# Optimization experiments

Hardware: AMD Instinct MI355X
Metric: run time of the kernel (lower is better)

Reference implementation:

```python
import jax, jax.numpy as jnp
import numpy as np


def rotate_half(x):
    d = x.shape[-1] // 2
    return jnp.concatenate([-x[..., d:], x[..., :d]], axis=-1)


def setup_inputs() -> dict:
    key = jax.random.key(0)
    ks = jax.random.split(key, 8)
    B, T, C, H = 2, 2048, 2048, 16
    hd = C // H
    x = jax.random.normal(ks[0], (B, T, C), dtype=jnp.float32)
    # realistic RoPE tables
    inv_freq = 1.0 / (10000.0 ** (jnp.arange(0, hd, 2, dtype=jnp.float32) / hd))
    t = jnp.arange(T, dtype=jnp.float32)
    freqs = jnp.einsum('t,f->tf', t, inv_freq)
    emb = jnp.concatenate([freqs, freqs], axis=-1)  # [T, hd]
    cos = jnp.cos(emb)
    sin = jnp.sin(emb)
    mask = jnp.tril(jnp.ones((T, T), dtype=bool))[None, None]  # causal [1,1,T,T]
    s = C ** -0.5
    Wq = jax.random.normal(ks[1], (C, C), dtype=jnp.float32) * s
    Wk = jax.random.normal(ks[2], (C, C), dtype=jnp.float32) * s
    Wv = jax.random.normal(ks[3], (C, C), dtype=jnp.float32) * s
    Wo = jax.random.normal(ks[4], (C, C), dtype=jnp.float32) * s
    return {"x": x, "cos": cos, "sin": sin, "mask": mask,
            "Wq": Wq, "Wk": Wk, "Wv": Wv, "Wo": Wo}


def reference(x, cos, sin, mask, Wq, Wk, Wv, Wo):
    B, T, C = x.shape
    H = 16
    hd = C // H
    scale = hd ** -0.5
    # projections: torch Linear stores W as [out,in], y = x @ W^T
    def proj(W):
        return jnp.einsum('btc,dc->btd', x, W).reshape(B, T, H, hd).transpose(0, 2, 1, 3)
    q, k, v = proj(Wq), proj(Wk), proj(Wv)  # [B,H,T,hd]
    c = cos[None, None]  # [1,1,T,hd]
    s = sin[None, None]
    q = q * c + rotate_half(q) * s
    k = k * c + rotate_half(k) * s
    attn = jnp.einsum('bhqd,bhkd->bhqk', q, k) * scale
    attn = jnp.where(mask, attn, -jnp.inf)
    attn = jax.nn.softmax(attn, axis=-1)
    out = jnp.einsum('bhqk,bhkd->bhqd', attn, v)
    out = out.transpose(0, 2, 1, 3).reshape(B, T, C)
    return jnp.einsum('btc,dc->btd', out, Wo)
```

## Files before the change

### kernel.cpp

```cpp
#include <hip/hip_runtime.h>
#include <cstdint>

typedef __bf16 bf16_t;
typedef __bf16 bf16x8 __attribute__((ext_vector_type(8)));
typedef __bf16 bf16x4 __attribute__((ext_vector_type(4)));
typedef float  f32x4  __attribute__((ext_vector_type(4)));

#define BB 2
#define TT 2048
#define CC 2048
#define HH 16
#define HD 128

static __device__ __forceinline__ void async_copy16(const void* gp, void* lp) {
  __builtin_amdgcn_global_load_lds(
      (const __attribute__((address_space(1))) void*)(uintptr_t)gp,
      (__attribute__((address_space(3))) void*)(uint32_t)(uintptr_t)lp,
      16, 0, 0);
}

__global__ __launch_bounds__(256)
void cast_all(const float* __restrict__ x, const float* __restrict__ wq,
              const float* __restrict__ wk, const float* __restrict__ wv,
              const float* __restrict__ wo, bf16_t* __restrict__ xb,
              bf16_t* __restrict__ wq_b) {
  const int NX4 = (BB * TT * CC) / 4;
  const int NW4 = (CC * CC) / 4;
  int i = blockIdx.x * 256 + threadIdx.x;
  const float* s;
  bf16_t* d;
  int off;
  if (i < NX4) {
    s = x; d = xb; off = i;
  } else {
    int j = i - NX4;
    int w = j >> 20;
    off = j & (NW4 - 1);
    s = (w == 0) ? wq : (w == 1) ? wk : (w == 2) ? wv : wo;
    d = wq_b + (size_t)w * (CC * CC);
  }
  float4 v = ((const float4*)s)[off];
  bf16x4 o;
  o[0] = (bf16_t)v.x; o[1] = (bf16_t)v.y; o[2] = (bf16_t)v.z; o[3] = (bf16_t)v.w;
  ((bf16x4*)d)[off] = o;
}

template <int MODE>
__global__ __launch_bounds__(256)
void gemm_bt(const bf16_t* __restrict__ A, const bf16_t* __restrict__ Bw,
             void* __restrict__ C0, void* __restrict__ C1, void* __restrict__ C2,
             int Kdim, int Ndim) {
  __shared__ __align__(16) char smem[128 * 136 * 2];
  bf16_t* As = (bf16_t*)smem;
  bf16_t* Bs = (bf16_t*)(smem + 16384);
  const int tid  = threadIdx.x;
  const int wave = tid >> 6, lane = tid & 63;
  const int quad = lane >> 4, l16 = lane & 15;
  const int m0 = blockIdx.y * 128, n0 = blockIdx.x * 128;
  const int wm = (wave >> 1) * 64, wn = (wave & 1) * 64;

  f32x4 acc[4][4] = {};

  const int srow = lane >> 3;
  const int scol = (((lane & 7) ^ srow) & 7) * 8;
  const int swz  = (l16 & 7) * 8;

  for (int k0 = 0; k0 < Kdim; k0 += 64) {
#pragma unroll
    for (int i = 0; i < 4; ++i) {
      int chunk = wave * 4 + i;
      int row = chunk * 8 + srow;
      async_copy16(A + (size_t)(m0 + row) * Kdim + k0 + scol, As + chunk * 512);
    }
#pragma unroll
    for (int i = 0; i < 4; ++i) {
      int chunk = wave * 4 + i;
      int row = chunk * 8 + srow;
      async_copy16(Bw + (size_t)(n0 + row) * Kdim + k0 + scol, Bs + chunk * 512);
    }
    __syncthreads();
#pragma unroll
    for (int kk = 0; kk < 64; kk += 32) {
      const int koff = (kk + quad * 8) ^ swz;
      bf16x8 af[4], bfr[4];
#pragma unroll
      for (int i = 0; i < 4; ++i)
        af[i] = *(const bf16x8*)&As[(wm + i * 16 + l16) * 64 + koff];
#pragma unroll
      for (int j = 0; j < 4; ++j)
        bfr[j] = *(const bf16x8*)&Bs[(wn + j * 16 + l16) * 64 + koff];
#pragma unroll
      for (int i = 0; i < 4; ++i)
#pragma unroll
        for (int j = 0; j < 4; ++j)
          acc[i][j] = __builtin_amdgcn_mfma_f32_16x16x32_bf16(af[i], bfr[j], acc[i][j], 0, 0, 0);
    }
    __syncthreads();
  }

  if (MODE == 0) {
#pragma unroll
    for (int i = 0; i < 4; ++i)
#pragma unroll
      for (int j = 0; j < 4; ++j) {
        int gcol = n0 + wn + j * 16 + l16;
#pragma unroll
        for (int r = 0; r < 4; ++r) {
          int grow = m0 + wm + i * 16 + quad * 4 + r;
          ((float*)C0)[(size_t)grow * Ndim + gcol] = acc[i][j][r];
        }
      }
  } else {
    const int proj = n0 >> 11;
    const int h = (n0 & (CC - 1)) >> 7;
    if (proj < 2) {
      bf16_t* dst = (bf16_t*)(proj == 0 ? C0 : C1);
#pragma unroll
      for (int i = 0; i < 4; ++i)
#pragma unroll
        for (int j = 0; j < 4; ++j) {
          int d = wn + j * 16 + l16;
#pragma unroll
          for (int r = 0; r < 4; ++r) {
            int grow = m0 + wm + i * 16 + quad * 4 + r;
            int b = grow >> 11, t = grow & (TT - 1);
            dst[(((size_t)(b * HH + h) * TT + t) * HD) + d] = (bf16_t)acc[i][j][r];
          }
        }
    } else {
      bf16_t* Ct = (bf16_t*)smem;
#pragma unroll
      for (int i = 0; i < 4; ++i)
#pragma unroll
        for (int j = 0; j < 4; ++j) {
          int c = wn + j * 16 + l16;
#pragma unroll
          for (int r = 0; r < 4; ++r)
            Ct[(wm + i * 16 + quad * 4 + r) * 136 + c] = (bf16_t)acc[i][j][r];
        }
      __syncthreads();
      const unsigned short* Cu = (const unsigned short*)Ct;
      int col = tid >> 1;
      int rh  = (tid & 1) * 64;
      int grow0 = m0 + rh;
      int b = grow0 >> 11, t0 = grow0 & (TT - 1);
      unsigned int pk[32];
#pragma unroll
      for (int s = 0; s < 32; ++s) {
        unsigned int lo = Cu[(rh + 2 * s) * 136 + col];
        unsigned int hi = Cu[(rh + 2 * s + 1) * 136 + col];
        pk[s] = lo | (hi << 16);
      }
      bf16_t* dstp = (bf16_t*)C2 + ((size_t)(b * HH + h) * HD + col) * TT + t0;
#pragma unroll
      for (int u = 0; u < 8; ++u) {
        uint4 w; w.x = pk[4*u]; w.y = pk[4*u+1]; w.z = pk[4*u+2]; w.w = pk[4*u+3];
        *(uint4*)(dstp + 8 * u) = w;
      }
    }
  }
}

__global__ __launch_bounds__(256) void rope_kernel(bf16_t* __restrict__ Q, bf16_t* __restrict__ K,
                                                   const float* __restrict__ cosT,
                                                   const float* __restrict__ sinT) {
  int idx = blockIdx.x * 256 + threadIdx.x;
  int d  = idx & 63;
  int t  = (idx >> 6) & (TT - 1);
  int bh = idx >> 17;
  size_t base = ((size_t)bh * TT + t) * HD;
  float c0 = cosT[t * HD + d],      s0 = sinT[t * HD + d];
  float c1 = cosT[t * HD + 64 + d], s1 = sinT[t * HD + 64 + d];
  float q0 = Q[base + d], q1 = Q[base + 64 + d];
  Q[base + d]      = (bf16_t)(q0 * c0 - q1 * s0);
  Q[base + 64 + d] = (bf16_t)(q1 * c1 + q0 * s1);
  float k0 = K[base + d], k1 = K[base + 64 + d];
  K[base + d]      = (bf16_t)(k0 * c0 - k1 * s0);
  K[base + 64 + d] = (bf16_t)(k1 * c1 + k0 * s1);
}

__global__ __launch_bounds__(256)
void attn_kernel(const bf16_t* __restrict__ Q, const bf16_t* __restrict__ K,
                 const bf16_t* __restrict__ Vt, bf16_t* __restrict__ Out) {
  __shared__ __align__(16) bf16_t Ks[2][64 * 128];
  __shared__ __align__(16) bf16_t Vs[2][128 * 64];
  __shared__ __align__(16) bf16_t Pl[4][2][16 * 72];
  const int lane = threadIdx.x & 63, wave = threadIdx.x >> 6;
  const int quad = lane >> 4, l16 = lane & 15;
  const int linear = blockIdx.x;
  const int hb = linear & 31;
  const int h = hb & (HH - 1), b = hb >> 4;
  const int qt = (TT / 128 - 1) - (linear >> 5);
  const int q0 = qt * 128 + wave * 32;
  const size_t qkbase = (size_t)(b * HH + h) * TT * HD;
  const bf16_t* Kh = K + qkbase;
  const bf16_t* Vh = Vt + (size_t)(b * HH + h) * HD * TT;
  const float scale = 0.08838834764831845f;

  const int srK = lane >> 4;
  const int sgK = lane & 15;
  const int scK0 = (sgK ^ srK) * 8;
  const int scK1 = (sgK ^ (4 + srK)) * 8;
  const int srV = lane >> 3;
  const int scV = (((lane & 7) ^ srV) & 7) * 8;
  const int swz = (l16 & 7) * 8;

  bf16x8 qf[2][4];
#pragma unroll
  for (int mt = 0; mt < 2; ++mt) {
    const bf16_t* qrow = Q + qkbase + (size_t)(q0 + mt * 16 + l16) * HD;
#pragma unroll
    for (int kc = 0; kc < 4; ++kc) qf[mt][kc] = *(const bf16x8*)(qrow + kc * 32 + quad * 8);
  }

  f32x4 o[2][8] = {};
  float l_i[2][4] = {};

  const int nIter = qt * 2 + 2;

  {
#pragma unroll
    for (int i = 0; i < 4; ++i) {
      int chunk = wave * 4 + i;
      int sc = (chunk & 1) ? scK1 : scK0;
      async_copy16(Kh + (size_t)(chunk * 4 + srK) * HD + sc, &Ks[0][chunk * 512]);
    }
#pragma unroll
    for (int i = 0; i < 4; ++i) {
      int chunk = wave * 4 + i;
      async_copy16(Vh + (size_t)(chunk * 8 + srV) * TT + scV, &Vs[0][chunk * 512]);
    }
  }

  for (int it = 0; it < nIter; ++it) {
    const int cur = it & 1;
    const int key0 = it * 64;
    __syncthreads();

    if (it + 1 < nIter) {
      const int nxt = cur ^ 1;
      const int knxt = key0 + 64;
#pragma unroll
      for (int i = 0; i < 4; ++i) {
        int chunk = wave * 4 + i;
        int sc = (chunk & 1) ? scK1 : scK0;
        async_copy16(Kh + (size_t)(knxt + chunk * 4 + srK) * HD + sc, &Ks[nxt][chunk * 512]);
      }
#pragma unroll
      for (int i = 0; i < 4; ++i) {
        int chunk = wave * 4 + i;
        async_copy16(Vh + (size_t)(chunk * 8 + srV) * TT + knxt + scV, &Vs[nxt][chunk * 512]);
      }
    }

    f32x4 s[2][4] = {};
#pragma unroll
    for (int kc = 0; kc < 4; ++kc) {
      const int koff = (kc * 32 + quad * 8) ^ swz;
#pragma unroll
      for (int kt = 0; kt < 4; ++kt) {
        bf16x8 kf = *(const bf16x8*)&Ks[cur][(kt * 16 + l16) * 128 + koff];
        s[0][kt] = __builtin_amdgcn_mfma_f32_16x16x32_bf16(qf[0][kc], kf, s[0][kt], 0, 0, 0);
        s[1][kt] = __builtin_amdgcn_mfma_f32_16x16x32_bf16(qf[1][kc], kf, s[1][kt], 0, 0, 0);
      }
    }

#pragma unroll
    for (int mt = 0; mt < 2; ++mt) {
      bf16_t* pl = &Pl[wave][mt][0];
#pragma unroll
      for (int r = 0; r < 4; ++r) {
        int rel = q0 + mt * 16 + quad * 4 + r - key0;
        int prow = (quad * 4 + r) * 72;
        float lr = 0.f;
#pragma unroll
        for (int kt = 0; kt < 4; ++kt) {
          int c16 = kt * 16 + l16;
          float e = (c16 > rel) ? 0.f : __expf(s[mt][kt][r] * scale);
          lr += e;
          pl[prow + c16] = (bf16_t)e;
        }
        l_i[mt][r] += lr;
      }
    }

    bf16x8 pf[2][2];
#pragma unroll
    for (int mt = 0; mt < 2; ++mt) {
      pf[mt][0] = *(const bf16x8*)&Pl[wave][mt][l16 * 72 + quad * 8];
      pf[mt][1] = *(const bf16x8*)&Pl[wave][mt][l16 * 72 + 32 + quad * 8];
    }
    const int voff0 = (quad * 8) ^ swz;
    const int voff1 = (32 + quad * 8) ^ swz;
#pragma unroll
    for (int n = 0; n < 8; ++n) {
      bf16x8 vf0 = *(const bf16x8*)&Vs[cur][(n * 16 + l16) * 64 + voff0];
      bf16x8 vf1 = *(const bf16x8*)&Vs[cur][(n * 16 + l16) * 64 + voff1];
      o[0][n] = __builtin_amdgcn_mfma_f32_16x16x32_bf16(pf[0][0], vf0, o[0][n], 0, 0, 0);
      o[0][n] = __builtin_amdgcn_mfma_f32_16x16x32_bf16(pf[0][1], vf1, o[0][n], 0, 0, 0);
      o[1][n] = __builtin_amdgcn_mfma_f32_16x16x32_bf16(pf[1][0], vf0, o[1][n], 0, 0, 0);
      o[1][n] = __builtin_amdgcn_mfma_f32_16x16x32_bf16(pf[1][1], vf1, o[1][n], 0, 0, 0);
    }
  }

#pragma unroll
  for (int mt = 0; mt < 2; ++mt)
#pragma unroll
    for (int r = 0; r < 4; ++r) {
      float l = l_i[mt][r];
#pragma unroll
      for (int off = 1; off < 16; off <<= 1) l += __shfl_xor(l, off);
      l_i[mt][r] = 1.f / l;
    }

#pragma unroll
  for (int mt = 0; mt < 2; ++mt)
#pragma unroll
    for (int n = 0; n < 8; ++n)
#pragma unroll
      for (int r = 0; r < 4; ++r) {
        int qg = q0 + mt * 16 + quad * 4 + r;
        size_t off = ((size_t)(b * TT + qg) * CC) + h * HD + n * 16 + l16;
        Out[off] = (bf16_t)(o[mt][n][r] * l_i[mt][r]);
      }
}

extern "C" void kernel_launch(void* const* d_in, const int* in_sizes, int n_in,
                              void* d_out, int out_size, void* d_ws, size_t ws_size,
                              hipStream_t stream) {
  const float* x    = (const float*)d_in[0];
  const float* cosT = (const float*)d_in[1];
  const float* sinT = (const float*)d_in[2];
  const float* Wq = (const float*)d_in[4];
  const float* Wk = (const float*)d_in[5];
  const float* Wv = (const float*)d_in[6];
  const float* Wo = (const float*)d_in[7];
  float* out = (float*)d_out;

  char* ws = (char*)d_ws;
  const size_t XSZ = (size_t)BB * TT * CC * 2;
  const size_t WSZ = (size_t)CC * CC * 2;
  bf16_t* x_bf  = (bf16_t*)(ws);
  bf16_t* wq_bf = (bf16_t*)(ws + XSZ);
  bf16_t* wo_bf = (bf16_t*)(ws + XSZ + 3 * WSZ);
  bf16_t* Qb    = (bf16_t*)(ws + XSZ + 4 * WSZ);
  bf16_t* Kb    = (bf16_t*)(ws + 2 * XSZ + 4 * WSZ);
  bf16_t* Vt    = (bf16_t*)(ws + 3 * XSZ + 4 * WSZ);
  bf16_t* attn_bf = x_bf;

  const int NX = BB * TT * CC;
  const int NW = CC * CC;
  cast_all<<<(NX / 4 + 4 * (NW / 4)) / 256, 256, 0, stream>>>(
      x, Wq, Wk, Wv, Wo, x_bf, wq_bf);

  gemm_bt<3><<<dim3(3 * CC / 128, BB * TT / 128), 256, 0, stream>>>(
      x_bf, wq_bf, Qb, Kb, Vt, CC, 3 * CC);

  rope_kernel<<<(BB * HH * TT * 64) / 256, 256, 0, stream>>>(Qb, Kb, cosT, sinT);

  attn_kernel<<<dim3(BB * HH * (TT / 128)), 256, 0, stream>>>(Qb, Kb, Vt, attn_bf);

  gemm_bt<0><<<dim3(CC / 128, BB * TT / 128), 256, 0, stream>>>(
      attn_bf, wo_bf, out, nullptr, nullptr, CC, CC);
}
```

Baseline: 394.8 us.

## Add 256x256-tile QKV GEMM with double-buffered async LDS and interleaved MFMA

Replaces the 128x128 templated QKV projection GEMM with a dedicated 512-thread kernel that computes 256x256 output tiles. It uses 128KB of dynamic LDS for double-buffered async global-to-LDS loads, interleaves the prefetch of the next stages with the MFMA groups, and raises wave priority around the MFMA blocks. The larger tile increases data reuse per load and cuts the number of K-loop barriers. In exchange it adds register pressure from 32 accumulators per lane and needs a two-pass LDS transpose for the V output. The generic GEMM is reduced to the fp32 output path.

```diff
diff --git a/kernel.cpp b/kernel.cpp
--- a/kernel.cpp
+++ b/kernel.cpp
@@ -98,60 +98,176 @@
     __syncthreads();
   }
 
-  if (MODE == 0) {
+#pragma unroll
+  for (int i = 0; i < 4; ++i)
+#pragma unroll
+    for (int j = 0; j < 4; ++j) {
+      int gcol = n0 + wn + j * 16 + l16;
+#pragma unroll
+      for (int r = 0; r < 4; ++r) {
+        int grow = m0 + wm + i * 16 + quad * 4 + r;
+        ((float*)C0)[(size_t)grow * Ndim + gcol] = acc[i][j][r];
+      }
+    }
+}
+
+__global__ __launch_bounds__(512, 2)
+void gemm_qkv256(const bf16_t* __restrict__ A, const bf16_t* __restrict__ Bw,
+                 bf16_t* __restrict__ Qo, bf16_t* __restrict__ Ko,
+                 bf16_t* __restrict__ Vo, int Kdim) {
+  extern __shared__ __align__(16) char smem[];
+  bf16_t* lds = (bf16_t*)smem;
+  const int tid  = threadIdx.x;
+  const int wave = tid >> 6, lane = tid & 63;
+  const int quad = lane >> 4, l16 = lane & 15;
+  const int wm = wave >> 2, wn = wave & 3;
+  const int n0 = blockIdx.x * 256, m0 = blockIdx.y * 256;
+
+  const int srow = lane >> 3;
+  const int scol = ((lane & 7) ^ srow) * 8;
+  const int swz  = (l16 & 7) * 8;
+  const int nK = Kdim >> 6;
+
+  const bf16_t* Ag = A  + (size_t)(m0 + wave * 32 + srow) * Kdim + scol;
+  const bf16_t* Bg = Bw + (size_t)(n0 + wave * 32 + srow) * Kdim + scol;
+  const int ldsChunk = wave * 4 * 512;
+
+#define STAGE_A(kt, buf)                                                      \
+  {                                                                           \
+    bf16_t* dstA = lds + (buf) * 32768 + ldsChunk;                            \
+    const bf16_t* srcA = Ag + (kt) * 64;                                      \
+    _Pragma("unroll")                                                         \
+    for (int ci = 0; ci < 4; ++ci)                                            \
+      async_copy16(srcA + (size_t)(ci * 8) * Kdim, dstA + ci * 512);          \
+  }
+#define STAGE_B(kt, buf)                                                      \
+  {                                                                           \
+    bf16_t* dstB = lds + (buf) * 32768 + 16384 + ldsChunk;                    \
+    const bf16_t* srcB = Bg + (kt) * 64;                                      \
+    _Pragma("unroll")                                                         \
+    for (int ci = 0; ci < 4; ++ci)                                            \
+      async_copy16(srcB + (size_t)(ci * 8) * Kdim, dstB + ci * 512);          \
+  }
+
+  f32x4 acc[8][4] = {};
+
+  STAGE_A(0, 0); STAGE_B(0, 0); STAGE_A(1, 1); STAGE_B(1, 1);
+
+  const int k0off = (quad * 8) ^ swz;
+  const int k1off = (32 + quad * 8) ^ swz;
+
+  for (int k = 0; k < nK; ++k) {
+    const int cur = k & 1;
+    const bf16_t* Asb = lds + cur * 32768;
+    const bf16_t* Bsb = Asb + 16384;
+    if (k < nK - 1) asm volatile("s_waitcnt vmcnt(8)" ::: "memory");
+    else            asm volatile("s_waitcnt vmcnt(0)" ::: "memory");
+    __builtin_amdgcn_s_barrier();
+    __builtin_amdgcn_sched_barrier(0);
+
+    bf16x8 a0[8], b0[4], a1[8], b1[4];
+#pragma unroll
+    for (int i = 0; i < 8; ++i)
+      a0[i] = *(const bf16x8*)&Asb[(wm * 128 + i * 16 + l16) * 64 + k0off];
+#pragma unroll
+    for (int j = 0; j < 4; ++j)
+      b0[j] = *(const bf16x8*)&Bsb[(wn * 64 + j * 16 + l16) * 64 + k0off];
+    asm volatile("s_waitcnt lgkmcnt(0)" ::: "memory");
+    __builtin_amdgcn_sched_barrier(0);
+    __builtin_amdgcn_s_setprio(1);
 #pragma unroll
     for (int i = 0; i < 4; ++i)
 #pragma unroll
+      for (int j = 0; j < 4; ++j)
+        acc[i][j] = __builtin_amdgcn_mfma_f32_16x16x32_bf16(a0[i], b0[j], acc[i][j], 0, 0, 0);
+    __builtin_amdgcn_s_setprio(0);
+
+#pragma unroll
+    for (int i = 0; i < 8; ++i)
+      a1[i] = *(const bf16x8*)&Asb[(wm * 128 + i * 16 + l16) * 64 + k1off];
+#pragma unroll
+    for (int j = 0; j < 4; ++j)
+      b1[j] = *(const bf16x8*)&Bsb[(wn * 64 + j * 16 + l16) * 64 + k1off];
+    __builtin_amdgcn_s_setprio(1);
+#pragma unroll
+    for (int i = 4; i < 8; ++i)
+#pragma unroll
+      for (int j = 0; j < 4; ++j)
+        acc[i][j] = __builtin_amdgcn_mfma_f32_16x16x32_bf16(a0[i], b0[j], acc[i][j], 0, 0, 0);
+    __builtin_amdgcn_s_setprio(0);
+    asm volatile("s_waitcnt lgkmcnt(0)" ::: "memory");
+    __builtin_amdgcn_s_barrier();
+    __builtin_amdgcn_sched_barrier(0);
+
+    if (k + 2 < nK) STAGE_A(k + 2, cur);
+    __builtin_amdgcn_s_setprio(1);
+#pragma unroll
+    for (int i = 0; i < 4; ++i)
+#pragma unroll
+      for (int j = 0; j < 4; ++j)
+        acc[i][j] = __builtin_amdgcn_mfma_f32_16x16x32_bf16(a1[i], b1[j], acc[i][j], 0, 0, 0);
+    __builtin_amdgcn_s_setprio(0);
+
+    if (k + 2 < nK) STAGE_B(k + 2, cur);
+    __builtin_amdgcn_s_setprio(1);
+#pragma unroll
+    for (int i = 4; i < 8; ++i)
+#pragma unroll
+      for (int j = 0; j < 4; ++j)
+        acc[i][j] = __builtin_amdgcn_mfma_f32_16x16x32_bf16(a1[i], b1[j], acc[i][j], 0, 0, 0);
+    __builtin_amdgcn_s_setprio(0);
+  }
+#undef STAGE_A
+#undef STAGE_B
+
+  const int proj = n0 >> 11;
+  if (proj < 2) {
+    bf16_t* dst = proj == 0 ? Qo : Ko;
+#pragma unroll
+    for (int i = 0; i < 8; ++i)
+#pragma unroll
       for (int j = 0; j < 4; ++j) {
-        int gcol = n0 + wn + j * 16 + l16;
+        int colv = (n0 & (CC - 1)) + wn * 64 + j * 16 + l16;
+        int h = colv >> 7, d = colv & (HD - 1);
 #pragma unroll
         for (int r = 0; r < 4; ++r) {
-          int grow = m0 + wm + i * 16 + quad * 4 + r;
-          ((float*)C0)[(size_t)grow * Ndim + gcol] = acc[i][j][r];
+          int grow = m0 + wm * 128 + i * 16 + quad * 4 + r;
+          int b = grow >> 11, t = grow & (TT - 1);
+          dst[(((size_t)(b * HH + h) * TT + t) * HD) + d] = (bf16_t)acc[i][j][r];
         }
       }
   } else {
-    const int proj = n0 >> 11;
-    const int h = (n0 & (CC - 1)) >> 7;
-    if (proj < 2) {
-      bf16_t* dst = (bf16_t*)(proj == 0 ? C0 : C1);
-#pragma unroll
-      for (int i = 0; i < 4; ++i)
-#pragma unroll
-        for (int j = 0; j < 4; ++j) {
-          int d = wn + j * 16 + l16;
-#pragma unroll
-          for (int r = 0; r < 4; ++r) {
-            int grow = m0 + wm + i * 16 + quad * 4 + r;
-            int b = grow >> 11, t = grow & (TT - 1);
-            dst[(((size_t)(b * HH + h) * TT + t) * HD) + d] = (bf16_t)acc[i][j][r];
+    bf16_t* Ct = (bf16_t*)smem;
+    const int b = m0 >> 11;
+#pragma unroll
+    for (int p = 0; p < 2; ++p) {
+      __syncthreads();
+      if (wm == p) {
+#pragma unroll
+        for (int i = 0; i < 8; ++i)
+#pragma unroll
+          for (int j = 0; j < 4; ++j) {
+            int c = wn * 64 + j * 16 + l16;
+#pragma unroll
+            for (int r = 0; r < 4; ++r)
+              Ct[(i * 16 + quad * 4 + r) * 264 + c] = (bf16_t)acc[i][j][r];
           }
-        }
-    } else {
-      bf16_t* Ct = (bf16_t*)smem;
-#pragma unroll
-      for (int i = 0; i < 4; ++i)
-#pragma unroll
-        for (int j = 0; j < 4; ++j) {
-          int c = wn + j * 16 + l16;
-#pragma unroll
-          for (int r = 0; r < 4; ++r)
-            Ct[(wm + i * 16 + quad * 4 + r) * 136 + c] = (bf16_t)acc[i][j][r];
-        }
+      }
       __syncthreads();
       const unsigned short* Cu = (const unsigned short*)Ct;
-      int col = tid >> 1;
-      int rh  = (tid & 1) * 64;
-      int grow0 = m0 + rh;
-      int b = grow0 >> 11, t0 = grow0 & (TT - 1);
+      int c  = tid & 255;
+      int rh = (tid >> 8) * 64;
+      int dv = (n0 & (CC - 1)) + c;
+      int h = dv >> 7, d = dv & (HD - 1);
       unsigned int pk[32];
 #pragma unroll
       for (int s = 0; s < 32; ++s) {
-        unsigned int lo = Cu[(rh + 2 * s) * 136 + col];
-        unsigned int hi = Cu[(rh + 2 * s + 1) * 136 + col];
+        unsigned int lo = Cu[(rh + 2 * s) * 264 + c];
+        unsigned int hi = Cu[(rh + 2 * s + 1) * 264 + c];
         pk[s] = lo | (hi << 16);
       }
-      bf16_t* dstp = (bf16_t*)C2 + ((size_t)(b * HH + h) * HD + col) * TT + t0;
+      bf16_t* dstp = Vo + ((size_t)(b * HH + h) * HD + d) * TT +
+                     (m0 & (TT - 1)) + p * 128 + rh;
 #pragma unroll
       for (int u = 0; u < 8; ++u) {
         uint4 w; w.x = pk[4*u]; w.y = pk[4*u+1]; w.z = pk[4*u+2]; w.w = pk[4*u+3];
@@ -353,8 +469,10 @@
   cast_all<<<(NX / 4 + 4 * (NW / 4)) / 256, 256, 0, stream>>>(
       x, Wq, Wk, Wv, Wo, x_bf, wq_bf);
 
-  gemm_bt<3><<<dim3(3 * CC / 128, BB * TT / 128), 256, 0, stream>>>(
-      x_bf, wq_bf, Qb, Kb, Vt, CC, 3 * CC);
+  (void)hipFuncSetAttribute(reinterpret_cast<const void*>(gemm_qkv256),
+                            hipFuncAttributeMaxDynamicSharedMemorySize, 131072);
+  gemm_qkv256<<<dim3(3 * CC / 256, BB * TT / 256), 512, 131072, stream>>>(
+      x_bf, wq_bf, Qb, Kb, Vt, CC);
 
   rope_kernel<<<(BB * HH * TT * 64) / 256, 256, 0, stream>>>(Qb, Kb, cosT, sinT);
 
```

Result: faster. 383.8 us (-2.8%).

## Add 256x256-tile double-buffered QKV GEMM kernel with interleaved async staging

Applied to the files above, without the earlier changes.

Replaces the 128x128 templated QKV projection GEMM with a dedicated 512-thread kernel using 256x256 tiles, 128KB of LDS double buffering, and a hand-scheduled phase loop that interleaves global-to-LDS async copies with MFMA groups under explicit waitcnt, barriers and setprio. The larger tile raises arithmetic intensity per loaded byte, and the software pipeline aims to hide load latency behind matrix math. The V transpose epilogue is split into two passes to fit the staging buffer. In exchange, the grid shrinks to 24x16 blocks, which may leave occupancy and wave balance worse across the GPU's compute units, and the manual scheduling is fragile.

```diff
diff --git a/kernel.cpp b/kernel.cpp
--- a/kernel.cpp
+++ b/kernel.cpp
@@ -98,60 +98,180 @@
     __syncthreads();
   }
 
-  if (MODE == 0) {
-#pragma unroll
-    for (int i = 0; i < 4; ++i)
+#pragma unroll
+  for (int i = 0; i < 4; ++i)
+#pragma unroll
+    for (int j = 0; j < 4; ++j) {
+      int gcol = n0 + wn + j * 16 + l16;
+#pragma unroll
+      for (int r = 0; r < 4; ++r) {
+        int grow = m0 + wm + i * 16 + quad * 4 + r;
+        ((float*)C0)[(size_t)grow * Ndim + gcol] = acc[i][j][r];
+      }
+    }
+}
+
+__global__ __launch_bounds__(512, 2)
+void gemm_qkv256(const bf16_t* __restrict__ A, const bf16_t* __restrict__ Bw,
+                 bf16_t* __restrict__ Qo, bf16_t* __restrict__ Ko,
+                 bf16_t* __restrict__ Vo, int Kdim) {
+  extern __shared__ __align__(16) char smem[];
+  bf16_t* lds = (bf16_t*)smem;
+  const int tid  = threadIdx.x;
+  const int wave = tid >> 6, lane = tid & 63;
+  const int quad = lane >> 4, l16 = lane & 15;
+  const int wm = wave >> 2, wn = wave & 3;
+  const int n0 = blockIdx.x * 256, m0 = blockIdx.y * 256;
+
+  const int srow = lane >> 3;
+  const int scol = ((lane & 7) ^ srow) * 8;
+  const int swz  = (l16 & 7) * 8;
+  const int nK = Kdim >> 6;
+  const int nPair = nK >> 1;
+
+  const bf16_t* Asrc = A  + (size_t)(m0 + srow) * Kdim + scol;
+  const bf16_t* Bsrc = Bw + (size_t)(n0 + srow) * Kdim + scol;
+
+#define STAGE_AH(BUF, H, KT) do {                                              \
+    bf16_t* d_ = lds + (BUF) * 32768 + (H) * 8192 + wave * 1024;               \
+    const bf16_t* s_ = Asrc + (size_t)((H) * 128 + wave * 16) * Kdim + (KT) * 64; \
+    async_copy16(s_, d_);                                                      \
+    async_copy16(s_ + (size_t)8 * Kdim, d_ + 512);                             \
+  } while (0)
+#define STAGE_BH(BUF, H, KT) do {                                              \
+    bf16_t* d_ = lds + (BUF) * 32768 + 16384 + (H) * 8192 + wave * 1024;       \
+    const bf16_t* s_ = Bsrc + (size_t)((H) * 128 + wave * 16) * Kdim + (KT) * 64; \
+    async_copy16(s_, d_);                                                      \
+    async_copy16(s_ + (size_t)8 * Kdim, d_ + 512);                             \
+  } while (0)
+
+  f32x4 acc[8][4] = {};
+  bf16x8 a[4][2], bfr[4][2];
+  const int k0off = (quad * 8) ^ swz;
+  const int k1off = (32 + quad * 8) ^ swz;
+
+#define RD_A(BUF, IH) { const bf16_t* Ab_ = lds + (BUF) * 32768;               \
+    _Pragma("unroll") for (int ii = 0; ii < 4; ++ii) {                         \
+      int ro = (wm * 128 + (IH) * 64 + ii * 16 + l16) * 64;                    \
+      a[ii][0] = *(const bf16x8*)&Ab_[ro + k0off];                             \
+      a[ii][1] = *(const bf16x8*)&Ab_[ro + k1off]; } }
+#define RD_B(BUF, JH) { const bf16_t* Bb_ = lds + (BUF) * 32768 + 16384;       \
+    _Pragma("unroll") for (int jj = 0; jj < 2; ++jj) {                         \
+      int ro = (wn * 64 + (JH) * 32 + jj * 16 + l16) * 64;                     \
+      bfr[(JH) * 2 + jj][0] = *(const bf16x8*)&Bb_[ro + k0off];                \
+      bfr[(JH) * 2 + jj][1] = *(const bf16x8*)&Bb_[ro + k1off]; } }
+#define MFMA16(IH, JH) {                                                       \
+    __builtin_amdgcn_s_setprio(1);                                             \
+    _Pragma("unroll") for (int ii = 0; ii < 4; ++ii)                           \
+    _Pragma("unroll") for (int jj = 0; jj < 2; ++jj) {                         \
+      acc[(IH) * 4 + ii][(JH) * 2 + jj] =                                      \
+          __builtin_amdgcn_mfma_f32_16x16x32_bf16(                             \
+              a[ii][0], bfr[(JH) * 2 + jj][0],                                 \
+              acc[(IH) * 4 + ii][(JH) * 2 + jj], 0, 0, 0);                     \
+      acc[(IH) * 4 + ii][(JH) * 2 + jj] =                                      \
+          __builtin_amdgcn_mfma_f32_16x16x32_bf16(                             \
+              a[ii][1], bfr[(JH) * 2 + jj][1],                                 \
+              acc[(IH) * 4 + ii][(JH) * 2 + jj], 0, 0, 0); }                   \
+    __builtin_amdgcn_s_setprio(0); }
+#define PH_MID() do { __builtin_amdgcn_s_barrier();                            \
+    asm volatile("s_waitcnt lgkmcnt(0)" ::: "memory");                         \
+    __builtin_amdgcn_sched_barrier(0); } while (0)
+#define PH_END() do { __builtin_amdgcn_sched_barrier(0);                       \
+    __builtin_amdgcn_s_barrier(); } while (0)
+#define KWAIT() do {                                                           \
+    if (i + 1 < nPair) asm volatile("s_waitcnt vmcnt(4)" ::: "memory");        \
+    else               asm volatile("s_waitcnt vmcnt(0)" ::: "memory");        \
+  } while (0)
+
+  STAGE_BH(0, 0, 0); STAGE_BH(0, 1, 0); STAGE_AH(0, 0, 0); STAGE_AH(0, 1, 0);
+  STAGE_BH(1, 0, 1); STAGE_BH(1, 1, 1);
+  asm volatile("s_waitcnt vmcnt(4)" ::: "memory");
+  __builtin_amdgcn_s_barrier();
+
+  for (int i = 0; i < nPair; ++i) {
+    const int T = 2 * i;
+    const bool mid  = (T + 2 < nK);
+    const bool tail = (T + 3 < nK);
+    RD_A(0, 0); RD_B(0, 0);
+    STAGE_AH(1, 0, T + 1);
+    PH_MID(); MFMA16(0, 0); PH_END();
+    RD_B(0, 1);
+    STAGE_AH(1, 1, T + 1);
+    PH_MID(); MFMA16(0, 1); PH_END();
+    RD_A(0, 1);
+    if (mid) STAGE_BH(0, 0, T + 2);
+    PH_MID(); MFMA16(1, 0); PH_END();
+    if (mid) STAGE_BH(0, 1, T + 2);
+    PH_MID(); MFMA16(1, 1); KWAIT(); PH_END();
+    RD_A(1, 0); RD_B(1, 0);
+    if (mid) STAGE_AH(0, 0, T + 2);
+    PH_MID(); MFMA16(0, 0); PH_END();
+    RD_B(1, 1);
+    if (mid) STAGE_AH(0, 1, T + 2);
+    PH_MID(); MFMA16(0, 1); PH_END();
+    RD_A(1, 1);
+    if (tail) STAGE_BH(1, 0, T + 3);
+    PH_MID(); MFMA16(1, 0); PH_END();
+    if (tail) STAGE_BH(1, 1, T + 3);
+    PH_MID(); MFMA16(1, 1); KWAIT(); PH_END();
+  }
+#undef STAGE_AH
+#undef STAGE_BH
+#undef RD_A
+#undef RD_B
+#undef MFMA16
+#undef PH_MID
+#undef PH_END
+#undef KWAIT
+
+  const int proj = n0 >> 11;
+  if (proj < 2) {
+    bf16_t* dst = proj == 0 ? Qo : Ko;
+#pragma unroll
+    for (int i = 0; i < 8; ++i)
 #pragma unroll
       for (int j = 0; j < 4; ++j) {
-        int gcol = n0 + wn + j * 16 + l16;
+        int colv = (n0 & (CC - 1)) + wn * 64 + j * 16 + l16;
+        int h = colv >> 7, d = colv & (HD - 1);
 #pragma unroll
         for (int r = 0; r < 4; ++r) {
-          int grow = m0 + wm + i * 16 + quad * 4 + r;
-          ((float*)C0)[(size_t)grow * Ndim + gcol] = acc[i][j][r];
+          int grow = m0 + wm * 128 + i * 16 + quad * 4 + r;
+          int b = grow >> 11, t = grow & (TT - 1);
+          dst[(((size_t)(b * HH + h) * TT + t) * HD) + d] = (bf16_t)acc[i][j][r];
         }
       }
   } else {
-    const int proj = n0 >> 11;
-    const int h = (n0 & (CC - 1)) >> 7;
-    if (proj < 2) {
-      bf16_t* dst = (bf16_t*)(proj == 0 ? C0 : C1);
-#pragma unroll
-      for (int i = 0; i < 4; ++i)
-#pragma unroll
-        for (int j = 0; j < 4; ++j) {
-          int d = wn + j * 16 + l16;
-#pragma unroll
-          for (int r = 0; r < 4; ++r) {
-            int grow = m0 + wm + i * 16 + quad * 4 + r;
-            int b = grow >> 11, t = grow & (TT - 1);
-            dst[(((size_t)(b * HH + h) * TT + t) * HD) + d] = (bf16_t)acc[i][j][r];
+    bf16_t* Ct = (bf16_t*)smem;
+    const int b = m0 >> 11;
+#pragma unroll
+    for (int p = 0; p < 2; ++p) {
+      __syncthreads();
+      if (wm == p) {
+#pragma unroll
+        for (int i = 0; i < 8; ++i)
+#pragma unroll
+          for (int j = 0; j < 4; ++j) {
+            int c = wn * 64 + j * 16 + l16;
+#pragma unroll
+            for (int r = 0; r < 4; ++r)
+              Ct[(i * 16 + quad * 4 + r) * 264 + c] = (bf16_t)acc[i][j][r];
           }
-        }
-    } else {
-      bf16_t* Ct = (bf16_t*)smem;
-#pragma unroll
-      for (int i = 0; i < 4; ++i)
-#pragma unroll
-        for (int j = 0; j < 4; ++j) {
-          int c = wn + j * 16 + l16;
-#pragma unroll
-          for (int r = 0; r < 4; ++r)
-            Ct[(wm + i * 16 + quad * 4 + r) * 136 + c] = (bf16_t)acc[i][j][r];
-        }
+      }
       __syncthreads();
       const unsigned short* Cu = (const unsigned short*)Ct;
-      int col = tid >> 1;
-      int rh  = (tid & 1) * 64;
-      int grow0 = m0 + rh;
-      int b = grow0 >> 11, t0 = grow0 & (TT - 1);
+      int c  = tid & 255;
+      int rh = (tid >> 8) * 64;
+      int dv = (n0 & (CC - 1)) + c;
+      int h = dv >> 7, d = dv & (HD - 1);
       unsigned int pk[32];
 #pragma unroll
       for (int s = 0; s < 32; ++s) {
-        unsigned int lo = Cu[(rh + 2 * s) * 136 + col];
-        unsigned int hi = Cu[(rh + 2 * s + 1) * 136 + col];
+        unsigned int lo = Cu[(rh + 2 * s) * 264 + c];
+        unsigned int hi = Cu[(rh + 2 * s + 1) * 264 + c];
         pk[s] = lo | (hi << 16);
       }
-      bf16_t* dstp = (bf16_t*)C2 + ((size_t)(b * HH + h) * HD + col) * TT + t0;
+      bf16_t* dstp = Vo + ((size_t)(b * HH + h) * HD + d) * TT +
+                     (m0 & (TT - 1)) + p * 128 + rh;
 #pragma unroll
       for (int u = 0; u < 8; ++u) {
         uint4 w; w.x = pk[4*u]; w.y = pk[4*u+1]; w.z = pk[4*u+2]; w.w = pk[4*u+3];
@@ -353,8 +473,10 @@
   cast_all<<<(NX / 4 + 4 * (NW / 4)) / 256, 256, 0, stream>>>(
       x, Wq, Wk, Wv, Wo, x_bf, wq_bf);
 
-  gemm_bt<3><<<dim3(3 * CC / 128, BB * TT / 128), 256, 0, stream>>>(
-      x_bf, wq_bf, Qb, Kb, Vt, CC, 3 * CC);
+  (void)hipFuncSetAttribute(reinterpret_cast<const void*>(gemm_qkv256),
+                            hipFuncAttributeMaxDynamicSharedMemorySize, 131072);
+  gemm_qkv256<<<dim3(3 * CC / 256, BB * TT / 256), 512, 131072, stream>>>(
+      x_bf, wq_bf, Qb, Kb, Vt, CC);
 
   rope_kernel<<<(BB * HH * TT * 64) / 256, 256, 0, stream>>>(Qb, Kb, cosT, sinT);
 
```

Measured after the change: 384.1 us. 1.03x faster.
